# Kernel optimization log

Hardware: AMD Instinct MI355X
Metric: run time of the kernel (lower is better)

## Reference

```python
import jax, jax.numpy as jnp
import numpy as np

INPUT_SIZE = 416.0
CONF_THRESH = 0.25
IOU_THRESH = 0.45
N = 8192


def setup_inputs() -> dict:
    key = jax.random.key(0)
    preds = jax.random.normal(key, (1, 5, N), dtype=jnp.float32)
    return {"preds": preds}


def _pairwise_iou(b):
    # b: [N,4] xyxy -> iou: [N,N], matching the torch clamp(min=0) semantics
    xx1 = jnp.maximum(b[:, None, 0], b[None, :, 0])
    yy1 = jnp.maximum(b[:, None, 1], b[None, :, 1])
    xx2 = jnp.minimum(b[:, None, 2], b[None, :, 2])
    yy2 = jnp.minimum(b[:, None, 3], b[None, :, 3])
    inter = jnp.clip(xx2 - xx1, 0.0) * jnp.clip(yy2 - yy1, 0.0)
    area = jnp.clip(b[:, 2] - b[:, 0], 0.0) * jnp.clip(b[:, 3] - b[:, 1], 0.0)  # [N]
    union = area[:, None] + area[None, :] - inter
    return jnp.where(union > 0, inter / union, 0.0)


def reference(preds):
    # decode: preds [1,5,N] rows = (cx, cy, w, h, obj)
    p = preds[0].T  # [N,5]
    cx, cy, pw, ph, obj = p[:, 0], p[:, 1], p[:, 2], p[:, 3], p[:, 4]
    x1 = cx - pw * 0.5
    y1 = cy - ph * 0.5
    x2 = cx + pw * 0.5
    y2 = cy + ph * 0.5
    boxes = jnp.stack([x1, y1, x2, y2], axis=1)  # [N,4]
    scores = obj
    classes = jnp.zeros_like(scores)

    valid = scores > CONF_THRESH  # conf filter (kept as mask; invalid boxes never kept)
    # scale to absolute coords iff all coords are normalized (max <= 1)
    scale = jnp.where(jnp.max(boxes) <= 1.0, INPUT_SIZE, 1.0)
    boxes_abs = boxes * scale

    # greedy NMS over score-descending order
    order = jnp.argsort(-scores)
    b = boxes_abs[order]          # [N,4]
    s = scores[order]             # [N]
    v = valid[order]              # [N]
    c = classes[order]            # [N]

    iou = _pairwise_iou(b)        # [N,N]

    def step(suppressed, xs):
        iou_row, v_i, i = xs
        keep_i = v_i & jnp.logical_not(suppressed[i])
        suppressed = suppressed | (keep_i & (iou_row > IOU_THRESH))
        return suppressed, keep_i

    _, keep = jax.lax.scan(
        step,
        jnp.zeros((N,), dtype=bool),
        (iou, v, jnp.arange(N)),
    )  # keep: [N] bool, in sorted order

    out = jnp.stack(
        [b[:, 0] / INPUT_SIZE, b[:, 1] / INPUT_SIZE,
         b[:, 2] / INPUT_SIZE, b[:, 3] / INPUT_SIZE, s, c],
        axis=1,
    )  # [N,6]
    # fixed-shape jit-compatible output: suppressed/filtered rows are zeroed;
    # kept rows appear in descending-score order (same order torch compacts to)
    return jnp.where(keep[:, None], out, 0.0)
```

## Files before the change

kernel.cpp:

```cpp
#include <hip/hip_runtime.h>
#include <stdint.h>

typedef unsigned long long u64;
typedef unsigned int u32;

#define NBOX 8192
#define ACMAX 1024
#define NCH 16
#define CONF 0.25f
#define IOU_T 0.45f

#define OFF_CX1    256
#define OFF_CY1    (OFF_CX1 + ACMAX * 4)
#define OFF_CX2    (OFF_CX1 + 2 * ACMAX * 4)
#define OFF_CY2    (OFF_CX1 + 3 * ACMAX * 4)
#define OFF_CSC    (OFF_CX1 + 4 * ACMAX * 4)
#define OFF_CAR    (OFF_CX1 + 5 * ACMAX * 4)
#define OFF_ROFC   (OFF_CX1 + 6 * ACMAX * 4)
#define OFF_CMASKT (OFF_CX1 + 7 * ACMAX * 4)

__device__ inline u64 readlane64(u64 v, int l) {
    u32 lo = (u32)__builtin_amdgcn_readlane((int)(u32)v, l);
    u32 hi = (u32)__builtin_amdgcn_readlane((int)(u32)(v >> 32), l);
    return ((u64)hi << 32) | (u64)lo;
}

__device__ inline u32 encf(float f) {
    u32 u = __float_as_uint(f);
    return (u & 0x80000000u) ? ~u : (u | 0x80000000u);
}

__global__ void __launch_bounds__(1024) k_sort(
        const float* __restrict__ p,
        float* __restrict__ cx1, float* __restrict__ cy1,
        float* __restrict__ cx2, float* __restrict__ cy2,
        float* __restrict__ csc, float* __restrict__ car,
        int* __restrict__ rofc, float* __restrict__ out) {
    #pragma clang fp contract(off)
    int t = threadIdx.x;
    int b = blockIdx.x;
    __shared__ u64 keys[1024];
    __shared__ u32 accs[128][36];
    __shared__ u32 accs2[8][32];
    __shared__ float redm[16];
    __shared__ float s_gmax;

    int il4 = (t & 7) * 4;
    int js  = t >> 3;
    int ibase = b * 32;

    u64 Ki[4];
    #pragma unroll
    for (int q = 0; q < 4; q++) {
        int i = ibase + il4 + q;
        u32 e = encf(p[4 * NBOX + i]);
        Ki[q] = ((u64)e << 32) | ((u64)(8191 - i) << 19) | 0x1FFFFull;
    }

    u32 acc[4] = {0u, 0u, 0u, 0u};
    float mloc = -3.4e38f;
    for (int w = 0; w < 8; w++) {
        int j = w * 1024 + t;
        float cxj = p[j], cyj = p[NBOX + j];
        float pwj = p[2 * NBOX + j], phj = p[3 * NBOX + j];
        float sj = p[4 * NBOX + j];
        float hx = pwj * 0.5f, hy = phj * 0.5f;
        float x1 = cxj - hx, y1 = cyj - hy, x2 = cxj + hx, y2 = cyj + hy;
        bool act = (sj > CONF) && (x2 > x1) && (y2 > y1);
        mloc = fmaxf(mloc, fmaxf(fmaxf(x1, y1), fmaxf(x2, y2)));
        u32 e = encf(sj);
        u32 mult = act ? 65537u : 1u;
        __syncthreads();
        keys[t] = ((u64)e << 32) | ((u64)(8191 - j) << 19) | (u64)mult;
        __syncthreads();
        int base = js * 8;
        #pragma unroll
        for (int k2 = 0; k2 < 4; k2++) {
            u64 ka = keys[base + k2 * 2];
            u64 kb = keys[base + k2 * 2 + 1];
            u32 ma = (u32)ka & 0x1FFFFu;
            u32 mb = (u32)kb & 0x1FFFFu;
            #pragma unroll
            for (int q = 0; q < 4; q++) {
                acc[q] += (ka > Ki[q]) ? ma : 0u;
                acc[q] += (kb > Ki[q]) ? mb : 0u;
            }
        }
    }
    #pragma unroll
    for (int q = 0; q < 4; q++) accs[js][il4 + q] = acc[q];
    #pragma unroll
    for (int o = 32; o > 0; o >>= 1) mloc = fmaxf(mloc, __shfl_xor(mloc, o, 64));
    if ((t & 63) == 0) redm[t >> 6] = mloc;
    __syncthreads();
    if (t < 256) {
        int il = t & 31, part = t >> 5;
        u32 s = 0;
        #pragma unroll
        for (int q = 0; q < 16; q++) s += accs[part * 16 + q][il];
        accs2[part][il] = s;
    }
    if (t == 0) {
        float g = redm[0];
        #pragma unroll
        for (int k = 1; k < 16; k++) g = fmaxf(g, redm[k]);
        s_gmax = g;
    }
    __syncthreads();
    if (t < 32) {
        u32 total = 0;
        #pragma unroll
        for (int part = 0; part < 8; part++) total += accs2[part][t];
        int r = (int)(total & 0xFFFFu);
        int cr = (int)(total >> 16);
        int i = ibase + t;
        float scale = (s_gmax <= 1.0f) ? 416.0f : 1.0f;
        float cx = p[i], cy = p[NBOX + i];
        float pw = p[2 * NBOX + i], ph = p[3 * NBOX + i];
        float s = p[4 * NBOX + i];
        float hx = pw * 0.5f, hy = ph * 0.5f;
        float x1 = cx - hx, y1 = cy - hy, x2 = cx + hx, y2 = cy + hy;
        bool a = (s > CONF) && (x2 > x1) && (y2 > y1);
        float bx1 = x1 * scale, by1 = y1 * scale;
        float bx2 = x2 * scale, by2 = y2 * scale;
        float aw = fmaxf(bx2 - bx1, 0.0f);
        float ah = fmaxf(by2 - by1, 0.0f);
        float area = aw * ah;
        bool ok = a && (cr < ACMAX);
        if (ok) {
            cx1[cr] = bx1; cy1[cr] = by1; cx2[cr] = bx2; cy2[cr] = by2;
            csc[cr] = s; car[cr] = area; rofc[cr] = r;
        } else {
            bool valid = s > CONF;
            float* o = out + (size_t)r * 6;
            o[0] = valid ? bx1 / 416.0f : 0.0f;
            o[1] = valid ? by1 / 416.0f : 0.0f;
            o[2] = valid ? bx2 / 416.0f : 0.0f;
            o[3] = valid ? by2 / 416.0f : 0.0f;
            o[4] = valid ? s : 0.0f;
            o[5] = 0.0f;
        }
    }
}

__global__ void __launch_bounds__(64) k_mask(
        const float* __restrict__ cx1, const float* __restrict__ cy1,
        const float* __restrict__ cx2, const float* __restrict__ cy2,
        const float* __restrict__ car, const float* __restrict__ csc,
        u64* __restrict__ cmaskT) {
    #pragma clang fp contract(off)
    int t = threadIdx.x;
    int i0 = blockIdx.x * 64, j0 = blockIdx.y * 64;
    u64 rv = __ballot(csc[i0 + t] > CONF);
    u64 cv = __ballot(csc[j0 + t] > CONF);
    if (rv == 0ull || cv == 0ull) return;
    __shared__ float sx1[64], sy1[64], sx2[64], sy2[64], sa[64];
    sx1[t] = cx1[i0 + t]; sy1[t] = cy1[i0 + t];
    sx2[t] = cx2[i0 + t]; sy2[t] = cy2[i0 + t];
    sa[t] = car[i0 + t];
    __syncthreads();
    int j = j0 + t;
    float xj1 = cx1[j], yj1 = cy1[j], xj2 = cx2[j], yj2 = cy2[j], aj = car[j];
    u64 w = 0;
    for (int ii = 0; ii < 64; ii++) {
        float xx1 = fmaxf(sx1[ii], xj1);
        float yy1 = fmaxf(sy1[ii], yj1);
        float xx2 = fminf(sx2[ii], xj2);
        float yy2 = fminf(sy2[ii], yj2);
        float iw = fmaxf(xx2 - xx1, 0.0f);
        float ih = fmaxf(yy2 - yy1, 0.0f);
        float inter = iw * ih;
        float uni = sa[ii] + aj - inter;
        bool sup = (uni > 0.0f) && (inter / uni > IOU_T);
        w |= ((u64)(sup ? 1u : 0u)) << ii;
    }
    cmaskT[(size_t)blockIdx.x * ACMAX + j] = w;
}

__global__ void __launch_bounds__(1024) k_final(
        const float* __restrict__ csc, const u64* __restrict__ cmaskT,
        const float* __restrict__ cx1, const float* __restrict__ cy1,
        const float* __restrict__ cx2, const float* __restrict__ cy2,
        const int* __restrict__ rofc, float* __restrict__ out) {
    int t = threadIdx.x;
    __shared__ u64 keptArr[NCH];
    int wv = t >> 6;
    float s = csc[t];
    bool valid = s > CONF;
    u64 col[NCH];
    #pragma unroll
    for (int w = 0; w < NCH; w++) col[w] = cmaskT[(size_t)w * ACMAX + t];
    bool sup = false;
    for (int c = 0; c < NCH; c++) {
        if (wv == c) {
            u64 validm = __ballot(valid);
            u64 supm = __ballot(sup);
            u64 d = col[c];
            u64 kept = 0;
            u64 cand = validm & ~supm;
            while (cand) {
                int i = __builtin_ctzll(cand);
                kept |= (1ull << i);
                u64 row = readlane64(d, i);
                u64 gt = (i < 63) ? (~0ull << (i + 1)) : 0ull;
                cand = cand & ~row & gt;
            }
            if ((t & 63) == 0) keptArr[c] = kept;
        }
        __syncthreads();
        u64 k = keptArr[c];
        if (wv > c && (col[c] & k) != 0ull) sup = true;
    }
    __syncthreads();
    if (valid) {
        bool kb = (keptArr[t >> 6] >> (t & 63)) & 1ull;
        int r = rofc[t];
        float* o = out + (size_t)r * 6;
        o[0] = kb ? cx1[t] / 416.0f : 0.0f;
        o[1] = kb ? cy1[t] / 416.0f : 0.0f;
        o[2] = kb ? cx2[t] / 416.0f : 0.0f;
        o[3] = kb ? cy2[t] / 416.0f : 0.0f;
        o[4] = kb ? s : 0.0f;
        o[5] = 0.0f;
    }
}

extern "C" void kernel_launch(void* const* d_in, const int* in_sizes, int n_in,
                              void* d_out, int out_size, void* d_ws, size_t ws_size,
                              hipStream_t stream) {
    const float* preds = (const float*)d_in[0];
    float* out = (float*)d_out;
    char* ws = (char*)d_ws;
    float* cx1 = (float*)(ws + OFF_CX1);
    float* cy1 = (float*)(ws + OFF_CY1);
    float* cx2 = (float*)(ws + OFF_CX2);
    float* cy2 = (float*)(ws + OFF_CY2);
    float* csc = (float*)(ws + OFF_CSC);
    float* car = (float*)(ws + OFF_CAR);
    int* rofc  = (int*)(ws + OFF_ROFC);
    u64* cmaskT = (u64*)(ws + OFF_CMASKT);

    hipLaunchKernelGGL(k_sort, dim3(256), dim3(1024), 0, stream,
                       preds, cx1, cy1, cx2, cy2, csc, car, rofc, out);
    hipLaunchKernelGGL(k_mask, dim3(NCH, NCH), dim3(64), 0, stream,
                       cx1, cy1, cx2, cy2, car, csc, cmaskT);
    hipLaunchKernelGGL(k_final, dim3(1), dim3(1024), 0, stream,
                       csc, cmaskT, cx1, cy1, cx2, cy2, rofc, out);
}
```

Measured before the change: 102.2 us.

## Fuse IoU mask and greedy NMS kernels using last-block atomic counter

Merges the mask-building kernel and the single-block final NMS kernel into one launch. Each of 16 blocks computes one row-chunk of the suppression mask for all 1024 candidates, then increments a global counter, and the last block to finish runs the greedy scan and writes the output. The counter is reset inside the sort kernel. This removes one kernel launch and its gap, but drops the early exit for tiles with no valid boxes, so the fused kernel computes every tile, and it relies on fences for cross-block visibility.

```diff
diff --git a/kernel.cpp b/kernel.cpp
--- a/kernel.cpp
+++ b/kernel.cpp
@@ -10,6 +10,7 @@
 #define CONF 0.25f
 #define IOU_T 0.45f
 
+#define OFF_CNT    0
 #define OFF_CX1    256
 #define OFF_CY1    (OFF_CX1 + ACMAX * 4)
 #define OFF_CX2    (OFF_CX1 + 2 * ACMAX * 4)
@@ -35,7 +36,8 @@
         float* __restrict__ cx1, float* __restrict__ cy1,
         float* __restrict__ cx2, float* __restrict__ cy2,
         float* __restrict__ csc, float* __restrict__ car,
-        int* __restrict__ rofc, float* __restrict__ out) {
+        int* __restrict__ rofc, u32* __restrict__ cnt0,
+        float* __restrict__ out) {
     #pragma clang fp contract(off)
     int t = threadIdx.x;
     int b = blockIdx.x;
@@ -44,6 +46,8 @@
     __shared__ u32 accs2[8][32];
     __shared__ float redm[16];
     __shared__ float s_gmax;
+
+    if (b == 0 && t == 0) *cnt0 = 0u;
 
     int il4 = (t & 7) * 4;
     int js  = t >> 3;
@@ -143,49 +147,56 @@
     }
 }
 
-__global__ void __launch_bounds__(64) k_mask(
+__global__ void __launch_bounds__(1024) k_nms2(
         const float* __restrict__ cx1, const float* __restrict__ cy1,
         const float* __restrict__ cx2, const float* __restrict__ cy2,
         const float* __restrict__ car, const float* __restrict__ csc,
-        u64* __restrict__ cmaskT) {
+        const int* __restrict__ rofc, u64* __restrict__ cmaskT,
+        u32* __restrict__ cnt, float* __restrict__ out) {
     #pragma clang fp contract(off)
     int t = threadIdx.x;
-    int i0 = blockIdx.x * 64, j0 = blockIdx.y * 64;
-    u64 rv = __ballot(csc[i0 + t] > CONF);
-    u64 cv = __ballot(csc[j0 + t] > CONF);
-    if (rv == 0ull || cv == 0ull) return;
+    int ci = blockIdx.x;
     __shared__ float sx1[64], sy1[64], sx2[64], sy2[64], sa[64];
-    sx1[t] = cx1[i0 + t]; sy1[t] = cy1[i0 + t];
-    sx2[t] = cx2[i0 + t]; sy2[t] = cy2[i0 + t];
-    sa[t] = car[i0 + t];
-    __syncthreads();
-    int j = j0 + t;
-    float xj1 = cx1[j], yj1 = cy1[j], xj2 = cx2[j], yj2 = cy2[j], aj = car[j];
-    u64 w = 0;
-    for (int ii = 0; ii < 64; ii++) {
-        float xx1 = fmaxf(sx1[ii], xj1);
-        float yy1 = fmaxf(sy1[ii], yj1);
-        float xx2 = fminf(sx2[ii], xj2);
-        float yy2 = fminf(sy2[ii], yj2);
-        float iw = fmaxf(xx2 - xx1, 0.0f);
-        float ih = fmaxf(yy2 - yy1, 0.0f);
-        float inter = iw * ih;
-        float uni = sa[ii] + aj - inter;
-        bool sup = (uni > 0.0f) && (inter / uni > IOU_T);
-        w |= ((u64)(sup ? 1u : 0u)) << ii;
-    }
-    cmaskT[(size_t)blockIdx.x * ACMAX + j] = w;
-}
-
-__global__ void __launch_bounds__(1024) k_final(
-        const float* __restrict__ csc, const u64* __restrict__ cmaskT,
-        const float* __restrict__ cx1, const float* __restrict__ cy1,
-        const float* __restrict__ cx2, const float* __restrict__ cy2,
-        const int* __restrict__ rofc, float* __restrict__ out) {
-    int t = threadIdx.x;
     __shared__ u64 keptArr[NCH];
+    __shared__ int isLast;
+
+    if (t < 64) {
+        sx1[t] = cx1[ci * 64 + t]; sy1[t] = cy1[ci * 64 + t];
+        sx2[t] = cx2[ci * 64 + t]; sy2[t] = cy2[ci * 64 + t];
+        sa[t]  = car[ci * 64 + t];
+    }
+    __syncthreads();
+    float xj1 = cx1[t], yj1 = cy1[t], xj2 = cx2[t], yj2 = cy2[t];
+    float aj = car[t];
+    float s = csc[t];
+    {
+        u64 w = 0;
+        for (int ii = 0; ii < 64; ii++) {
+            float xx1 = fmaxf(sx1[ii], xj1);
+            float yy1 = fmaxf(sy1[ii], yj1);
+            float xx2 = fminf(sx2[ii], xj2);
+            float yy2 = fminf(sy2[ii], yj2);
+            float iw = fmaxf(xx2 - xx1, 0.0f);
+            float ih = fmaxf(yy2 - yy1, 0.0f);
+            float inter = iw * ih;
+            float uni = sa[ii] + aj - inter;
+            bool sup = (uni > 0.0f) && (inter / uni > IOU_T);
+            w |= ((u64)(sup ? 1u : 0u)) << ii;
+        }
+        cmaskT[(size_t)ci * ACMAX + t] = w;
+    }
+    __threadfence();
+    __syncthreads();
+    if (t == 0) {
+        u32 old = __hip_atomic_fetch_add(cnt, 1u, __ATOMIC_ACQ_REL,
+                                         __HIP_MEMORY_SCOPE_AGENT);
+        isLast = (old == (u32)(NCH - 1)) ? 1 : 0;
+    }
+    __syncthreads();
+    if (!isLast) return;
+    __threadfence();
+
     int wv = t >> 6;
-    float s = csc[t];
     bool valid = s > CONF;
     u64 col[NCH];
     #pragma unroll
@@ -216,10 +227,10 @@
         bool kb = (keptArr[t >> 6] >> (t & 63)) & 1ull;
         int r = rofc[t];
         float* o = out + (size_t)r * 6;
-        o[0] = kb ? cx1[t] / 416.0f : 0.0f;
-        o[1] = kb ? cy1[t] / 416.0f : 0.0f;
-        o[2] = kb ? cx2[t] / 416.0f : 0.0f;
-        o[3] = kb ? cy2[t] / 416.0f : 0.0f;
+        o[0] = kb ? xj1 / 416.0f : 0.0f;
+        o[1] = kb ? yj1 / 416.0f : 0.0f;
+        o[2] = kb ? xj2 / 416.0f : 0.0f;
+        o[3] = kb ? yj2 / 416.0f : 0.0f;
         o[4] = kb ? s : 0.0f;
         o[5] = 0.0f;
     }
@@ -231,6 +242,7 @@
     const float* preds = (const float*)d_in[0];
     float* out = (float*)d_out;
     char* ws = (char*)d_ws;
+    u32* cnt   = (u32*)(ws + OFF_CNT);
     float* cx1 = (float*)(ws + OFF_CX1);
     float* cy1 = (float*)(ws + OFF_CY1);
     float* cx2 = (float*)(ws + OFF_CX2);
@@ -241,9 +253,7 @@
     u64* cmaskT = (u64*)(ws + OFF_CMASKT);
 
     hipLaunchKernelGGL(k_sort, dim3(256), dim3(1024), 0, stream,
-                       preds, cx1, cy1, cx2, cy2, csc, car, rofc, out);
-    hipLaunchKernelGGL(k_mask, dim3(NCH, NCH), dim3(64), 0, stream,
-                       cx1, cy1, cx2, cy2, car, csc, cmaskT);
-    hipLaunchKernelGGL(k_final, dim3(1), dim3(1024), 0, stream,
-                       csc, cmaskT, cx1, cy1, cx2, cy2, rofc, out);
-}
+                       preds, cx1, cy1, cx2, cy2, csc, car, rofc, cnt, out);
+    hipLaunchKernelGGL(k_nms2, dim3(NCH), dim3(1024), 0, stream,
+                       cx1, cy1, cx2, cy2, car, csc, rofc, cmaskT, cnt, out);
+}
```

After: 111.2 us. +8.8%, slower.
